# Kernel tuning notes

Measured on AMD Instinct MI355X. Metric: run time of the kernel, lower is better.

The kernel has to match this reference:

```python
import jax, jax.numpy as jnp
import numpy as np

HEADS = 16
DIM_HEAD = 128
DIM = HEADS * DIM_HEAD          # hidden_size = 2048
SEGMENT_LEN = 496
NUM_LONGTERM = 16
NUM_PERSIST = 16
C = SEGMENT_LEN + NUM_LONGTERM  # total_segment_len = 512 (window width)
EPS = 1e-6
THETA = 10000.0
NEG = -jnp.finfo(jnp.float32).max


def _rope(t, cos, sin):
    # t: [b, h, n, d]; cos/sin: [n, d]; interleaved (rotate-half on adjacent pairs)
    t2 = t.reshape(t.shape[:-1] + (DIM_HEAD // 2, 2))
    rot = jnp.stack((-t2[..., 1], t2[..., 0]), axis=-1).reshape(t.shape)
    return t * cos + rot * sin


def _attn_bias():
    # queries: [m_len longterm-mem tokens | segment tokens]
    # keys:    [p_len persistent | m_len longterm-mem | segment tokens]
    q_len = C
    k_len = C + NUM_PERSIST
    pq = NUM_LONGTERM
    pk = NUM_PERSIST + NUM_LONGTERM
    bias = jnp.full((q_len, k_len), NEG, dtype=jnp.float32)
    bias = bias.at[:, :pk].set(0.0)  # everyone attends to the prefix
    sq = q_len - pq
    causal = jnp.tril(jnp.ones((sq, sq), dtype=bool))
    bias = bias.at[pq:, pk:].set(jnp.where(causal, 0.0, NEG))
    return bias


def setup_inputs() -> dict:
    key = jax.random.key(0)
    k1, k2, k3, k4 = jax.random.split(key, 4)
    b, n = 2, 4096  # n must be a multiple of C=512
    return {
        "x": jax.random.normal(k1, (b, n, DIM), dtype=jnp.float32),
        "norm_w": jnp.ones((DIM,), dtype=jnp.float32),
        "w_qkv": jax.random.normal(k2, (3 * DIM, DIM), dtype=jnp.float32) * 0.02,
        "w_out": jax.random.normal(k3, (DIM, DIM), dtype=jnp.float32) * 0.02,
        "pm": jax.random.normal(k4, (2, HEADS, NUM_PERSIST, DIM_HEAD), dtype=jnp.float32) * 0.02,
    }


def reference(x, norm_w, w_qkv, w_out, pm):
    b, n, d = x.shape
    # RMSNorm
    xn = x * jax.lax.rsqrt(jnp.mean(x * x, axis=-1, keepdims=True) + EPS) * norm_w
    # qkv projection (Linear, no bias)
    qkv = xn @ w_qkv.T
    q, k, v = jnp.split(qkv, 3, axis=-1)

    def to_heads(t):  # [b, n, h*d] -> [b, h, n, d]
        return t.reshape(b, n, HEADS, DIM_HEAD).transpose(0, 2, 1, 3)

    q, k, v = to_heads(q), to_heads(k), to_heads(v)

    # RoPE over full sequence positions 0..n-1 (before windowing)
    inv_freq = 1.0 / (THETA ** (jnp.arange(0, DIM_HEAD, 2, dtype=jnp.float32) / DIM_HEAD))
    freqs = jnp.arange(n, dtype=jnp.float32)[:, None] * inv_freq  # [n, d/2]
    freqs = jnp.repeat(freqs, 2, axis=-1)                          # [n, d]
    cos, sin = jnp.cos(freqs), jnp.sin(freqs)
    q = _rope(q, cos, sin)
    k = _rope(k, cos, sin)

    # split into windows of width C: [b, h, n, d] -> [(b*w), h, C, d]
    w = n // C

    def to_windows(t):
        return t.reshape(b, HEADS, w, C, DIM_HEAD).transpose(0, 2, 1, 3, 4).reshape(b * w, HEADS, C, DIM_HEAD)

    q, k, v = to_windows(q), to_windows(k), to_windows(v)

    # prepend persistent memory tokens to k, v
    pmk = jnp.broadcast_to(pm[0], (b * w, HEADS, NUM_PERSIST, DIM_HEAD))
    pmv = jnp.broadcast_to(pm[1], (b * w, HEADS, NUM_PERSIST, DIM_HEAD))
    k = jnp.concatenate((pmk, k), axis=-2)  # [(b*w), h, C+P, d]
    v = jnp.concatenate((pmv, v), axis=-2)

    bias = _attn_bias()  # [C, C+P]
    scale = DIM_HEAD ** -0.5
    sim = jnp.einsum('whqd,whkd->whqk', q, k) * scale + bias
    attn = jax.nn.softmax(sim, axis=-1)
    out = jnp.einsum('whqk,whkd->whqd', attn, v)

    # '(b w) h c d -> b (w c) (h d)'
    out = out.reshape(b, w, HEADS, C, DIM_HEAD).transpose(0, 1, 3, 2, 4).reshape(b, n, HEADS * DIM_HEAD)
    return out @ w_out.T
```

## Files before the change

kernel.cpp:

```cpp
#include <hip/hip_runtime.h>
#include <hip/hip_bf16.h>

typedef __attribute__((ext_vector_type(8))) short short8v;
typedef __attribute__((ext_vector_type(4))) float f32x4;
typedef __attribute__((ext_vector_type(4))) unsigned short us4;

#define DEV static __device__ __forceinline__

DEV unsigned short f2bf(float f) {
  unsigned u = __builtin_bit_cast(unsigned, f);
  u += 0x7FFFu + ((u >> 16) & 1u);
  return (unsigned short)(u >> 16);
}
DEV float bf2f(unsigned short s) {
  unsigned u = ((unsigned)s) << 16;
  return __builtin_bit_cast(float, u);
}
DEV void gload16(const void* g, void* l) {
  __builtin_amdgcn_global_load_lds((const __attribute__((address_space(1))) void*)g,
                                   (__attribute__((address_space(3))) void*)l, 16, 0, 0);
}

__global__ __launch_bounds__(256) void k_cvt(const float* __restrict__ s,
                                             unsigned short* __restrict__ d, long n4) {
  long i = (long)blockIdx.x * 256 + threadIdx.x;
  if (i >= n4) return;
  f32x4 v = *((const f32x4*)s + i);
  us4 o;
  o[0] = f2bf(v[0]); o[1] = f2bf(v[1]); o[2] = f2bf(v[2]); o[3] = f2bf(v[3]);
  *((us4*)d + i) = o;
}

__global__ __launch_bounds__(256) void k_pmprep(const float* __restrict__ pm,
                                                unsigned short* __restrict__ pmk,
                                                unsigned short* __restrict__ vt,
                                                unsigned short* __restrict__ zbuf) {
  int idx = blockIdx.x * 256 + threadIdx.x;
  if (idx < 8) zbuf[idx] = 0;
  if (idx >= 16 * 16 * 128) return;
  int d = idx & 127, p = (idx >> 7) & 15, h = idx >> 11;
  float kvl = pm[((0 * 16 + h) * 16 + p) * 128 + d];
  float vvl = pm[((1 * 16 + h) * 16 + p) * 128 + d];
  pmk[(h * 16 + p) * 128 + d] = f2bf(kvl);
  unsigned short vb = f2bf(vvl);
  for (int w = 0; w < 16; ++w) {
    long base = ((long)(w * 16 + h) * 128 + d) * 576;
    vt[base + p] = vb;
    vt[base + 528 + p] = 0;
    vt[base + 544 + p] = 0;
    vt[base + 560 + p] = 0;
  }
}

__global__ __launch_bounds__(256) void k_ropetab(float* __restrict__ ct, float* __restrict__ st) {
  int idx = blockIdx.x * 256 + threadIdx.x;
  int pos = idx >> 6, i = idx & 63;
  float invf = __powf(10000.f, -(float)i * (1.f / 64.f));
  float a = (float)pos * invf;
  ct[idx] = cosf(a);
  st[idx] = sinf(a);
}

__global__ __launch_bounds__(256) void k_rms(const float* __restrict__ x,
                                             const float* __restrict__ w,
                                             unsigned short* __restrict__ xb) {
  int row = blockIdx.x, tid = threadIdx.x;
  const f32x4* xr = (const f32x4*)(x + (long)row * 2048);
  f32x4 v0 = xr[tid * 2], v1 = xr[tid * 2 + 1];
  float ss = v0[0]*v0[0] + v0[1]*v0[1] + v0[2]*v0[2] + v0[3]*v0[3]
           + v1[0]*v1[0] + v1[1]*v1[1] + v1[2]*v1[2] + v1[3]*v1[3];
  ss += __shfl_xor(ss, 1);  ss += __shfl_xor(ss, 2);  ss += __shfl_xor(ss, 4);
  ss += __shfl_xor(ss, 8);  ss += __shfl_xor(ss, 16); ss += __shfl_xor(ss, 32);
  __shared__ float red[4];
  if ((tid & 63) == 0) red[tid >> 6] = ss;
  __syncthreads();
  float tot = red[0] + red[1] + red[2] + red[3];
  float rs = rsqrtf(tot * (1.f / 2048.f) + 1e-6f);
  float xv[8] = {v0[0], v0[1], v0[2], v0[3], v1[0], v1[1], v1[2], v1[3]};
  short8v pack;
#pragma unroll
  for (int j = 0; j < 8; ++j) pack[j] = (short)f2bf(xv[j] * rs * w[tid * 8 + j]);
  *((short8v*)(xb + (long)row * 2048) + tid) = pack;
}


#define VMCNT4 asm volatile("s_waitcnt vmcnt(4)" ::: "memory")
#define VMCNT0 asm volatile("s_waitcnt vmcnt(0)" ::: "memory")
#define SCHEDB __builtin_amdgcn_sched_barrier(0)
#define NOSTG ((void)0)

template <int OUTF32>
__global__ __launch_bounds__(512, 2) void k_gemm8(const unsigned short* __restrict__ A,
                                                  const unsigned short* __restrict__ B,
                                                  unsigned short* __restrict__ Cb,
                                                  float* __restrict__ Cf,
                                                  int M, int N, int K) {
  __shared__ __align__(16) unsigned short lds[4 * 256 * 64];
  const int tid = threadIdx.x;
  const int lane = tid & 63;
  const int ql = lane & 15, g = lane >> 4;
  const int wid = tid >> 6;
  const int wm = wid >> 2, wn = wid & 3;

  const int nbx = N >> 8;
  const int nwg = gridDim.x;
  int bid = blockIdx.x;
  int swz = (bid & 7) * (nwg >> 3) + (bid >> 3);
  int by = swz / nbx, bx = swz - by * nbx;
  const long rowA0 = (long)by << 8;
  const long rowB0 = (long)bx << 8;

  const int idx0 = tid, idx1 = 512 + tid;
  const int dr0 = idx0 >> 3, sc0 = (idx0 & 7) ^ (dr0 & 7);
  const int dr1 = idx1 >> 3, sc1 = (idx1 & 7) ^ (dr1 & 7);
  const long halfA = 128L * K;
  const unsigned short* pA0 = A + (rowA0 + dr0) * (long)K + sc0 * 8;
  const unsigned short* pA1 = A + (rowA0 + dr1) * (long)K + sc1 * 8;
  const unsigned short* pB0 = B + (rowB0 + dr0) * (long)K + sc0 * 8;
  const unsigned short* pB1 = B + (rowB0 + dr1) * (long)K + sc1 * 8;

  const int rsw0 = (g ^ (ql & 7)) * 8;
  const int rsw1 = ((4 + g) ^ (ql & 7)) * 8;

  short8v fa[4], fb[2][4];
  f32x4 acc[8][4] = {};

#define STAGE_A(b, h, kk) do { \
  gload16(pA0 + (long)(h) * halfA + (kk), lds + (b) * 32768 + (h) * 8192 + (idx0 << 3)); \
  gload16(pA1 + (long)(h) * halfA + (kk), lds + (b) * 32768 + (h) * 8192 + (idx1 << 3)); } while (0)
#define STAGE_B(b, h, kk) do { \
  gload16(pB0 + (long)(h) * halfA + (kk), lds + (b) * 32768 + 16384 + (h) * 8192 + (idx0 << 3)); \
  gload16(pB1 + (long)(h) * halfA + (kk), lds + (b) * 32768 + 16384 + (h) * 8192 + (idx1 << 3)); } while (0)

#define PHASE(buf, mh, ks, LOADB, STG, VMC) do { \
  { const unsigned short* p_ = lds + (buf) * 32768 + (((wm << 7) + (mh) * 64 + ql) << 6) + ((ks) ? rsw1 : rsw0); \
    _Pragma("unroll") for (int mi_ = 0; mi_ < 4; ++mi_) fa[mi_] = *(const short8v*)(p_ + (mi_ << 10)); } \
  if (LOADB) { const unsigned short* p_ = lds + (buf) * 32768 + 16384 + (((wn << 6) + ql) << 6) + ((ks) ? rsw1 : rsw0); \
    _Pragma("unroll") for (int n_ = 0; n_ < 4; ++n_) fb[ks][n_] = *(const short8v*)(p_ + (n_ << 10)); } \
  STG; \
  SCHEDB; __builtin_amdgcn_s_barrier(); SCHEDB; \
  __builtin_amdgcn_s_setprio(1); \
  _Pragma("unroll") for (int mi_ = 0; mi_ < 4; ++mi_) \
    _Pragma("unroll") for (int n_ = 0; n_ < 4; ++n_) \
      acc[(mh) * 4 + mi_][n_] = __builtin_amdgcn_mfma_f32_16x16x32_bf16(fa[mi_], fb[ks][n_], acc[(mh) * 4 + mi_][n_], 0, 0, 0); \
  __builtin_amdgcn_s_setprio(0); \
  VMC; \
  SCHEDB; __builtin_amdgcn_s_barrier(); SCHEDB; \
} while (0)

  const int NT = K >> 6;
  const int NITER = NT >> 1;

  STAGE_A(0, 0, 0); STAGE_A(0, 1, 0);
  STAGE_B(0, 0, 0); STAGE_B(0, 1, 0);
  STAGE_B(1, 0, 64); STAGE_B(1, 1, 64);
  VMCNT4;
  SCHEDB; __builtin_amdgcn_s_barrier(); SCHEDB;

  for (int i = 0; i < NITER - 1; ++i) {
    const int k1 = (2 * i + 1) << 6;
    const int k2 = (2 * i + 2) << 6;
    const int k3 = (2 * i + 3) << 6;
    PHASE(0, 0, 0, 1, STAGE_A(1, 0, k1), NOSTG);
    PHASE(0, 0, 1, 1, STAGE_A(1, 1, k1), NOSTG);
    PHASE(0, 1, 0, 0, STAGE_B(0, 0, k2), NOSTG);
    PHASE(0, 1, 1, 0, STAGE_B(0, 1, k2), VMCNT4);
    PHASE(1, 0, 0, 1, STAGE_A(0, 0, k2), NOSTG);
    PHASE(1, 0, 1, 1, STAGE_A(0, 1, k2), NOSTG);
    PHASE(1, 1, 0, 0, STAGE_B(1, 0, k3), NOSTG);
    PHASE(1, 1, 1, 0, STAGE_B(1, 1, k3), VMCNT4);
  }
  {
    const int k1 = (NT - 1) << 6;
    PHASE(0, 0, 0, 1, STAGE_A(1, 0, k1), NOSTG);
    PHASE(0, 0, 1, 1, STAGE_A(1, 1, k1), NOSTG);
    PHASE(0, 1, 0, 0, NOSTG, NOSTG);
    PHASE(0, 1, 1, 0, NOSTG, VMCNT0);
    PHASE(1, 0, 0, 1, NOSTG, NOSTG);
    PHASE(1, 0, 1, 1, NOSTG, NOSTG);
    PHASE(1, 1, 0, 0, NOSTG, NOSTG);
    PHASE(1, 1, 1, 0, NOSTG, NOSTG);
  }

#pragma unroll
  for (int am = 0; am < 8; ++am)
#pragma unroll
    for (int n = 0; n < 4; ++n)
#pragma unroll
      for (int r = 0; r < 4; ++r) {
        long row = rowA0 + (wm << 7) + am * 16 + (g << 2) + r;
        long col = rowB0 + (wn << 6) + n * 16 + ql;
        if (OUTF32) Cf[row * N + col] = acc[am][n][r];
        else        Cb[row * N + col] = f2bf(acc[am][n][r]);
      }
#undef STAGE_A
#undef STAGE_B
#undef PHASE
}

__global__ __launch_bounds__(256) void k_kprep(unsigned short* __restrict__ qkv,
                                               unsigned short* __restrict__ vt,
                                               const float* __restrict__ ct,
                                               const float* __restrict__ st) {
  __shared__ unsigned short lt[64 * 136];
  const int tile = blockIdx.x, h = blockIdx.y;
  const int tid = threadIdx.x;
  const int t0 = tile * 64;
  {
    int row = t0 + (tid >> 2);
    int d0 = (tid & 3) * 32;
    int pos = row & 4095;
    unsigned short* kp = qkv + (long)row * 6144 + 2048 + h * 128 + d0;
    const float* cp = ct + pos * 64 + (d0 >> 1);
    const float* sp = st + pos * 64 + (d0 >> 1);
    f32x4 cv[4], sv[4];
#pragma unroll
    for (int j = 0; j < 4; ++j) { cv[j] = *(const f32x4*)(cp + j * 4); sv[j] = *(const f32x4*)(sp + j * 4); }
    short8v kv[4];
#pragma unroll
    for (int j = 0; j < 4; ++j) kv[j] = *(const short8v*)(kp + j * 8);
#pragma unroll
    for (int j = 0; j < 4; ++j) {
      short8v outv;
#pragma unroll
      for (int p = 0; p < 4; ++p) {
        float a = bf2f((unsigned short)kv[j][2 * p]);
        float b = bf2f((unsigned short)kv[j][2 * p + 1]);
        float c = cv[j][p], s = sv[j][p];
        outv[2 * p]     = (short)f2bf(a * c - b * s);
        outv[2 * p + 1] = (short)f2bf(b * c + a * s);
      }
      *(short8v*)(kp + j * 8) = outv;
    }
  }
  {
    int row = tid >> 2, seg = tid & 3;
    const unsigned short* src = qkv + (long)(t0 + row) * 6144 + 4096 + h * 128 + seg * 32;
#pragma unroll
    for (int j = 0; j < 4; ++j)
      *(short8v*)(lt + row * 136 + seg * 32 + j * 8) = *(const short8v*)(src + j * 8);
  }
  __syncthreads();
  int d = tid >> 1, half = tid & 1;
  int wh = t0 >> 9;
  long dst = ((long)(wh * 16 + h) * 128 + d) * 576 + (t0 & 511) + 16 + half * 32;
  unsigned short tmp[32];
#pragma unroll
  for (int kk = 0; kk < 32; ++kk) tmp[kk] = lt[(half * 32 + kk) * 136 + d];
#pragma unroll
  for (int j = 0; j < 4; ++j) {
    short8v v;
#pragma unroll
    for (int e = 0; e < 8; ++e) v[e] = (short)tmp[j * 8 + e];
    *(short8v*)(vt + dst + j * 8) = v;
  }
}

__global__ __launch_bounds__(512, 4) void k_attn(const unsigned short* __restrict__ qkv,
                                                 const unsigned short* __restrict__ vt,
                                                 const unsigned short* __restrict__ pmk,
                                                 const unsigned short* __restrict__ zbuf,
                                                 const float* __restrict__ ct,
                                                 const float* __restrict__ stt,
                                                 unsigned short* __restrict__ attno) {
  __shared__ __align__(16) unsigned short Ks[2][64 * 128];
  __shared__ __align__(16) unsigned short Vs[2][128 * 64];
  const int qb = blockIdx.x, wh = blockIdx.y, h = blockIdx.z;
  const int tid = threadIdx.x;
  const int wave = tid >> 6, lane = tid & 63;
  const int ql = lane & 15, g = lane >> 4;
  const int tokbase = (wh >> 3) * 4096 + (wh & 7) * 512;
  const int qi = qb * 128 + wave * 16 + ql;
  const int wqmax = qb * 128 + wave * 16 + 15;
  const long qrow = (long)(tokbase + qi) * 6144;
  const int pos = (tokbase + qi) & 4095;
  short8v qf[4];
#pragma unroll
  for (int ks = 0; ks < 4; ++ks) {
    short8v qv = *(const short8v*)(qkv + qrow + h * 128 + ks * 32 + g * 8);
    f32x4 cv = *(const f32x4*)(ct + pos * 64 + ks * 16 + g * 4);
    f32x4 sv = *(const f32x4*)(stt + pos * 64 + ks * 16 + g * 4);
    const float SC = 0.08838834764831845f;
#pragma unroll
    for (int p = 0; p < 4; ++p) {
      float a = bf2f((unsigned short)qv[2 * p]);
      float b = bf2f((unsigned short)qv[2 * p + 1]);
      qf[ks][2 * p]     = (short)f2bf((a * cv[p] - b * sv[p]) * SC);
      qf[ks][2 * p + 1] = (short)f2bf((b * cv[p] + a * sv[p]) * SC);
    }
  }
  const int nkt = (qb * 128 + 144 + 63) >> 6;
  const long vbase = (long)(wh * 16 + h) * 128 * 576;

  float mrun = -3.0e38f, lrun = 0.f;
  f32x4 o[8] = {};

#define STAGEKV(kt, b) do { \
    _Pragma("unroll") for (int i2 = 0; i2 < 2; ++i2) { \
      int idx_ = i2 * 512 + tid; \
      int kl_ = idx_ >> 4, dc_ = idx_ & 15, dcs_ = dc_ ^ (kl_ & 7); \
      int ki_ = (kt) * 64 + kl_; \
      const unsigned short* src_; \
      if (ki_ < 16)       src_ = pmk + (h * 16 + ki_) * 128 + dcs_ * 8; \
      else if (ki_ < 528) src_ = qkv + (long)(tokbase + ki_ - 16) * 6144 + 2048 + h * 128 + dcs_ * 8; \
      else                src_ = zbuf; \
      gload16(src_, &Ks[b][0] + (size_t)idx_ * 8); } \
    _Pragma("unroll") for (int i2 = 0; i2 < 2; ++i2) { \
      int idx_ = i2 * 512 + tid; \
      int d_ = idx_ >> 3, kc_ = idx_ & 7, kcs_ = kc_ ^ (d_ & 7); \
      gload16(vt + vbase + (long)d_ * 576 + (kt) * 64 + kcs_ * 8, &Vs[b][0] + (size_t)idx_ * 8); } \
  } while (0)

  STAGEKV(0, 0);
  __syncthreads();
  for (int kt = 0; kt < nkt; ++kt) {
    const int cur = kt & 1;
    if (kt + 1 < nkt) STAGEKV(kt + 1, cur ^ 1);
    if (kt * 64 <= wqmax + 16) {
      f32x4 stv[4] = {};
      __builtin_amdgcn_s_setprio(1);
#pragma unroll
      for (int kf = 0; kf < 4; ++kf) {
        int row = kf * 16 + ql;
#pragma unroll
        for (int ks = 0; ks < 4; ++ks) {
          int chunk = (ks * 4 + g) ^ (row & 7);
          short8v kv = *(const short8v*)(&Ks[cur][0] + row * 128 + chunk * 8);
          stv[kf] = __builtin_amdgcn_mfma_f32_16x16x32_bf16(kv, qf[ks], stv[kf], 0, 0, 0);
        }
      }
      __builtin_amdgcn_s_setprio(0);
      float tmax = -3.0e38f;
#pragma unroll
      for (int kf = 0; kf < 4; ++kf)
#pragma unroll
        for (int r = 0; r < 4; ++r) {
          int ki = kt * 64 + kf * 16 + g * 4 + r;
          bool ok = (ki < 32) || (qi >= 16 && ki <= qi + 16);
          float s = ok ? stv[kf][r] : -3.0e38f;
          stv[kf][r] = s;
          tmax = fmaxf(tmax, s);
        }
      tmax = fmaxf(tmax, __shfl_xor(tmax, 16));
      tmax = fmaxf(tmax, __shfl_xor(tmax, 32));
      if (!__all(tmax <= mrun + 8.f)) {
        float mnew = fmaxf(mrun, tmax);
        float corr = __expf(mrun - mnew);
        lrun *= corr;
#pragma unroll
        for (int db = 0; db < 8; ++db) {
          o[db][0] *= corr; o[db][1] *= corr; o[db][2] *= corr; o[db][3] *= corr;
        }
        mrun = mnew;
      }
      float psum = 0.f;
#pragma unroll
      for (int kf = 0; kf < 4; ++kf)
#pragma unroll
        for (int r = 0; r < 4; ++r) {
          float p = __expf(stv[kf][r] - mrun);
          stv[kf][r] = p;
          psum += p;
        }
      psum += __shfl_xor(psum, 16);
      psum += __shfl_xor(psum, 32);
      lrun += psum;
      short8v pb[2];
#pragma unroll
      for (int kc2 = 0; kc2 < 2; ++kc2)
#pragma unroll
        for (int j = 0; j < 8; ++j) {
          int srcl = (((g & 1) * 2 + (j >> 2)) << 4) | ql;
          float v0 = __shfl(stv[kc2 * 2][j & 3], srcl);
          float v1 = __shfl(stv[kc2 * 2 + 1][j & 3], srcl);
          pb[kc2][j] = (short)f2bf((g >> 1) ? v1 : v0);
        }
      __builtin_amdgcn_s_setprio(1);
#pragma unroll
      for (int db = 0; db < 8; ++db) {
        int d = db * 16 + ql;
#pragma unroll
        for (int kc2 = 0; kc2 < 2; ++kc2) {
          int chunk = (kc2 * 4 + g) ^ (d & 7);
          short8v vf = *(const short8v*)(&Vs[cur][0] + d * 64 + chunk * 8);
          o[db] = __builtin_amdgcn_mfma_f32_16x16x32_bf16(vf, pb[kc2], o[db], 0, 0, 0);
        }
      }
      __builtin_amdgcn_s_setprio(0);
    }
    __syncthreads();
  }
#undef STAGEKV
  float inv = 1.0f / lrun;
  long obase = (long)(tokbase + qi) * 2048 + h * 128;
#pragma unroll
  for (int db = 0; db < 8; ++db)
#pragma unroll
    for (int r = 0; r < 4; ++r)
      attno[obase + db * 16 + g * 4 + r] = f2bf(o[db][r] * inv);
}

extern "C" void kernel_launch(void* const* d_in, const int* in_sizes, int n_in,
                              void* d_out, int out_size, void* d_ws, size_t ws_size,
                              hipStream_t stream) {
  const float* x      = (const float*)d_in[0];
  const float* norm_w = (const float*)d_in[1];
  const float* w_qkv  = (const float*)d_in[2];
  const float* w_out  = (const float*)d_in[3];
  const float* pm     = (const float*)d_in[4];
  float* out = (float*)d_out;

  char* ws = (char*)d_ws;
  size_t off = 0;
  auto alloc = [&](size_t bytes) -> void* {
    void* p = ws + off;
    off += (bytes + 255) & ~(size_t)255;
    return p;
  };
  unsigned short* xb    = (unsigned short*)alloc(8192ull * 2048 * 2);
  unsigned short* wqkvb = (unsigned short*)alloc(6144ull * 2048 * 2);
  unsigned short* woutb = (unsigned short*)alloc(2048ull * 2048 * 2);
  unsigned short* qkv   = (unsigned short*)alloc(8192ull * 6144 * 2);
  unsigned short* vt    = (unsigned short*)alloc(256ull * 128 * 576 * 2);
  unsigned short* attno = (unsigned short*)alloc(8192ull * 2048 * 2);
  unsigned short* pmk   = (unsigned short*)alloc(16 * 16 * 128 * 2);
  float* ct             = (float*)alloc(4096 * 64 * 4);
  float* stt            = (float*)alloc(4096 * 64 * 4);
  unsigned short* zbuf  = (unsigned short*)alloc(256);

  hipLaunchKernelGGL(k_cvt, dim3(12288), dim3(256), 0, stream, w_qkv, wqkvb, 3145728L);
  hipLaunchKernelGGL(k_cvt, dim3(4096), dim3(256), 0, stream, w_out, woutb, 1048576L);
  hipLaunchKernelGGL(k_pmprep, dim3(128), dim3(256), 0, stream, pm, pmk, vt, zbuf);
  hipLaunchKernelGGL(k_ropetab, dim3(1024), dim3(256), 0, stream, ct, stt);
  hipLaunchKernelGGL(k_rms, dim3(8192), dim3(256), 0, stream, x, norm_w, xb);
  hipLaunchKernelGGL((k_gemm8<0>), dim3(24 * 32), dim3(512), 0, stream,
                     xb, wqkvb, qkv, (float*)nullptr, 8192, 6144, 2048);
  hipLaunchKernelGGL(k_kprep, dim3(128, 16), dim3(256), 0, stream, qkv, vt, ct, stt);
  hipLaunchKernelGGL(k_attn, dim3(4, 16, 16), dim3(512), 0, stream,
                     qkv, vt, pmk, zbuf, ct, stt, attno);
  hipLaunchKernelGGL((k_gemm8<1>), dim3(8 * 32), dim3(512), 0, stream,
                     attno, woutb, (unsigned short*)nullptr, out, 8192, 2048, 2048);
}
```

Before: 423.4 us.

## Shrink attention KV tile to 32 keys and skip masking on interior tiles

Halves the key/value tile from 64 to 32 keys, which halves shared memory per block and lets more blocks fit per CU (the min-blocks launch bound is also dropped). The finer tile means less masked-out work past the causal diagonal, since loop count and per-wave skip now work at 32-key granularity. Mask evaluation is skipped for tiles that sit fully inside the causal region. The cost is twice as many barriers and staging rounds per block, and each tile carries less MFMA work to hide load latency.

```diff
diff --git a/kernel.cpp b/kernel.cpp
--- a/kernel.cpp
+++ b/kernel.cpp
@@ -256,22 +256,23 @@
   }
 }
 
-__global__ __launch_bounds__(512, 4) void k_attn(const unsigned short* __restrict__ qkv,
-                                                 const unsigned short* __restrict__ vt,
-                                                 const unsigned short* __restrict__ pmk,
-                                                 const unsigned short* __restrict__ zbuf,
-                                                 const float* __restrict__ ct,
-                                                 const float* __restrict__ stt,
-                                                 unsigned short* __restrict__ attno) {
-  __shared__ __align__(16) unsigned short Ks[2][64 * 128];
-  __shared__ __align__(16) unsigned short Vs[2][128 * 64];
+__global__ __launch_bounds__(512) void k_attn(const unsigned short* __restrict__ qkv,
+                                              const unsigned short* __restrict__ vt,
+                                              const unsigned short* __restrict__ pmk,
+                                              const unsigned short* __restrict__ zbuf,
+                                              const float* __restrict__ ct,
+                                              const float* __restrict__ stt,
+                                              unsigned short* __restrict__ attno) {
+  __shared__ __align__(16) unsigned short Ks[2][32 * 128];
+  __shared__ __align__(16) unsigned short Vs[2][128 * 32];
   const int qb = blockIdx.x, wh = blockIdx.y, h = blockIdx.z;
   const int tid = threadIdx.x;
   const int wave = tid >> 6, lane = tid & 63;
   const int ql = lane & 15, g = lane >> 4;
   const int tokbase = (wh >> 3) * 4096 + (wh & 7) * 512;
   const int qi = qb * 128 + wave * 16 + ql;
-  const int wqmax = qb * 128 + wave * 16 + 15;
+  const int wqmin = qb * 128 + wave * 16;
+  const int wqmax = wqmin + 15;
   const long qrow = (long)(tokbase + qi) * 6144;
   const int pos = (tokbase + qi) & 4095;
   short8v qf[4];
@@ -289,26 +290,22 @@
       qf[ks][2 * p + 1] = (short)f2bf((b * cv[p] + a * sv[p]) * SC);
     }
   }
-  const int nkt = (qb * 128 + 144 + 63) >> 6;
+  const int nkt = min(17, (qb * 128 + 144 + 31) >> 5);
   const long vbase = (long)(wh * 16 + h) * 128 * 576;
 
   float mrun = -3.0e38f, lrun = 0.f;
   f32x4 o[8] = {};
 
 #define STAGEKV(kt, b) do { \
-    _Pragma("unroll") for (int i2 = 0; i2 < 2; ++i2) { \
-      int idx_ = i2 * 512 + tid; \
-      int kl_ = idx_ >> 4, dc_ = idx_ & 15, dcs_ = dc_ ^ (kl_ & 7); \
-      int ki_ = (kt) * 64 + kl_; \
+    { int kl_ = tid >> 4, dc_ = tid & 15, dcs_ = dc_ ^ (kl_ & 7); \
+      int ki_ = (kt) * 32 + kl_; \
       const unsigned short* src_; \
       if (ki_ < 16)       src_ = pmk + (h * 16 + ki_) * 128 + dcs_ * 8; \
       else if (ki_ < 528) src_ = qkv + (long)(tokbase + ki_ - 16) * 6144 + 2048 + h * 128 + dcs_ * 8; \
       else                src_ = zbuf; \
-      gload16(src_, &Ks[b][0] + (size_t)idx_ * 8); } \
-    _Pragma("unroll") for (int i2 = 0; i2 < 2; ++i2) { \
-      int idx_ = i2 * 512 + tid; \
-      int d_ = idx_ >> 3, kc_ = idx_ & 7, kcs_ = kc_ ^ (d_ & 7); \
-      gload16(vt + vbase + (long)d_ * 576 + (kt) * 64 + kcs_ * 8, &Vs[b][0] + (size_t)idx_ * 8); } \
+      gload16(src_, &Ks[b][0] + (size_t)tid * 8); } \
+    { int d_ = tid >> 2, kc_ = tid & 3, kcs_ = kc_ ^ (d_ & 3); \
+      gload16(vt + vbase + (long)d_ * 576 + (kt) * 32 + kcs_ * 8, &Vs[b][0] + (size_t)tid * 8); } \
   } while (0)
 
   STAGEKV(0, 0);
@@ -316,11 +313,11 @@
   for (int kt = 0; kt < nkt; ++kt) {
     const int cur = kt & 1;
     if (kt + 1 < nkt) STAGEKV(kt + 1, cur ^ 1);
-    if (kt * 64 <= wqmax + 16) {
-      f32x4 stv[4] = {};
+    if (kt * 32 <= wqmax + 16) {
+      f32x4 stv[2] = {};
       __builtin_amdgcn_s_setprio(1);
 #pragma unroll
-      for (int kf = 0; kf < 4; ++kf) {
+      for (int kf = 0; kf < 2; ++kf) {
         int row = kf * 16 + ql;
 #pragma unroll
         for (int ks = 0; ks < 4; ++ks) {
@@ -331,16 +328,24 @@
       }
       __builtin_amdgcn_s_setprio(0);
       float tmax = -3.0e38f;
-#pragma unroll
-      for (int kf = 0; kf < 4; ++kf)
-#pragma unroll
-        for (int r = 0; r < 4; ++r) {
-          int ki = kt * 64 + kf * 16 + g * 4 + r;
-          bool ok = (ki < 32) || (qi >= 16 && ki <= qi + 16);
-          float s = ok ? stv[kf][r] : -3.0e38f;
-          stv[kf][r] = s;
-          tmax = fmaxf(tmax, s);
-        }
+      const bool needmask = !(kt == 0 || (kt * 32 + 15 <= wqmin));
+      if (needmask) {
+#pragma unroll
+        for (int kf = 0; kf < 2; ++kf)
+#pragma unroll
+          for (int r = 0; r < 4; ++r) {
+            int ki = kt * 32 + kf * 16 + g * 4 + r;
+            bool ok = (ki < 32) || (qi >= 16 && ki <= qi + 16);
+            float s = ok ? stv[kf][r] : -3.0e38f;
+            stv[kf][r] = s;
+            tmax = fmaxf(tmax, s);
+          }
+      } else {
+#pragma unroll
+        for (int kf = 0; kf < 2; ++kf)
+#pragma unroll
+          for (int r = 0; r < 4; ++r) tmax = fmaxf(tmax, stv[kf][r]);
+      }
       tmax = fmaxf(tmax, __shfl_xor(tmax, 16));
       tmax = fmaxf(tmax, __shfl_xor(tmax, 32));
       if (!__all(tmax <= mrun + 8.f)) {
@@ -355,7 +360,7 @@
       }
       float psum = 0.f;
 #pragma unroll
-      for (int kf = 0; kf < 4; ++kf)
+      for (int kf = 0; kf < 2; ++kf)
 #pragma unroll
         for (int r = 0; r < 4; ++r) {
           float p = __expf(stv[kf][r] - mrun);
@@ -365,26 +370,21 @@
       psum += __shfl_xor(psum, 16);
       psum += __shfl_xor(psum, 32);
       lrun += psum;
-      short8v pb[2];
-#pragma unroll
-      for (int kc2 = 0; kc2 < 2; ++kc2)
-#pragma unroll
-        for (int j = 0; j < 8; ++j) {
-          int srcl = (((g & 1) * 2 + (j >> 2)) << 4) | ql;
-          float v0 = __shfl(stv[kc2 * 2][j & 3], srcl);
-          float v1 = __shfl(stv[kc2 * 2 + 1][j & 3], srcl);
-          pb[kc2][j] = (short)f2bf((g >> 1) ? v1 : v0);
-        }
+      short8v pb;
+#pragma unroll
+      for (int j = 0; j < 8; ++j) {
+        int srcl = (((g & 1) * 2 + (j >> 2)) << 4) | ql;
+        float v0 = __shfl(stv[0][j & 3], srcl);
+        float v1 = __shfl(stv[1][j & 3], srcl);
+        pb[j] = (short)f2bf((g >> 1) ? v1 : v0);
+      }
       __builtin_amdgcn_s_setprio(1);
 #pragma unroll
       for (int db = 0; db < 8; ++db) {
         int d = db * 16 + ql;
-#pragma unroll
-        for (int kc2 = 0; kc2 < 2; ++kc2) {
-          int chunk = (kc2 * 4 + g) ^ (d & 7);
-          short8v vf = *(const short8v*)(&Vs[cur][0] + d * 64 + chunk * 8);
-          o[db] = __builtin_amdgcn_mfma_f32_16x16x32_bf16(vf, pb[kc2], o[db], 0, 0, 0);
-        }
+        int kc = g ^ (d & 3);
+        short8v vf = *(const short8v*)(&Vs[cur][0] + d * 32 + kc * 8);
+        o[db] = __builtin_amdgcn_mfma_f32_16x16x32_bf16(vf, pb, o[db], 0, 0, 0);
       }
       __builtin_amdgcn_s_setprio(0);
     }
```

Measured after the change: 428.5 us. About the same (+1.2%).
